# Kernel tuning notes

Measured on AMD Instinct MI355X. Metric: run time of the kernel, lower is better.

The kernel has to match this reference:

```python
import jax, jax.numpy as jnp
import numpy as np

N_HEAD = 16

def setup_inputs() -> dict:
    key = jax.random.key(0)
    k1, k2, k3 = jax.random.split(key, 3)
    B, T, C = 2, 2048, 2048
    x = jax.random.normal(k1, (B, T, C), dtype=jnp.float32)
    # torch Linear weights are [out, in]; init with small scale for stability
    w_attn = jax.random.normal(k2, (3 * C, C), dtype=jnp.float32) * 0.02
    b_attn = jnp.zeros((3 * C,), dtype=jnp.float32)
    w_proj = jax.random.normal(k3, (C, C), dtype=jnp.float32) * 0.02
    b_proj = jnp.zeros((C,), dtype=jnp.float32)
    return {"x": x, "w_attn": w_attn, "b_attn": b_attn, "w_proj": w_proj, "b_proj": b_proj}

def reference(x, w_attn, b_attn, w_proj, b_proj):
    B, T, C = x.shape
    nh = N_HEAD
    hs = C // nh
    # fused QKV projection (torch Linear: x @ W^T + b)
    qkv = x @ w_attn.T + b_attn                      # [B, T, 3C]
    q, k, v = jnp.split(qkv, 3, axis=2)
    # [B, nh, T, hs]
    q = q.reshape(B, T, nh, hs).transpose(0, 2, 1, 3)
    k = k.reshape(B, T, nh, hs).transpose(0, 2, 1, 3)
    v = v.reshape(B, T, nh, hs).transpose(0, 2, 1, 3)
    # causal scaled dot-product attention
    scale = 1.0 / jnp.sqrt(jnp.asarray(hs, dtype=x.dtype))
    logits = jnp.einsum("bhqd,bhkd->bhqk", q, k) * scale  # [B, nh, T, T]
    causal = jnp.tril(jnp.ones((T, T), dtype=bool))
    logits = jnp.where(causal, logits, jnp.finfo(logits.dtype).min)
    attn = jax.nn.softmax(logits, axis=-1)
    y = jnp.einsum("bhqk,bhkd->bhqd", attn, v)       # [B, nh, T, hs]
    y = y.transpose(0, 2, 1, 3).reshape(B, T, C)
    # output projection (resid_dropout is identity in eval / p=0)
    y = y @ w_proj.T + b_proj
    return y
```

## Files before the change

### kernel.cpp

```cpp
#include <hip/hip_runtime.h>
#include <stdint.h>

typedef __bf16 bf16_t;
typedef __bf16 bf16x8 __attribute__((ext_vector_type(8)));
typedef float f32x4 __attribute__((ext_vector_type(4)));
typedef unsigned short us16x8 __attribute__((ext_vector_type(8)));

#define MFMA16(a, b, c) __builtin_amdgcn_mfma_f32_16x16x32_bf16(a, b, c, 0, 0, 0)
#define BAR() __builtin_amdgcn_s_barrier()
#define PRIO1() __builtin_amdgcn_s_setprio(1)
#define PRIO0() __builtin_amdgcn_s_setprio(0)
#define LGKM0()                                        \
  do {                                                 \
    asm volatile("s_waitcnt lgkmcnt(0)" ::: "memory"); \
    __builtin_amdgcn_sched_barrier(0);                 \
  } while (0)
#define VMCNT(n)                                          \
  do {                                                    \
    asm volatile("s_waitcnt vmcnt(" #n ")" ::: "memory"); \
    __builtin_amdgcn_sched_barrier(0);                    \
  } while (0)

__device__ __forceinline__ void stage16(const bf16_t* g, bf16_t* l) {
  __builtin_amdgcn_global_load_lds((__attribute__((address_space(1))) void*)g,
                                   (__attribute__((address_space(3))) void*)l, 16, 0, 0);
}

__global__ __launch_bounds__(256) void cvt_f32_to_bf16(const float* __restrict__ in,
                                                       bf16_t* __restrict__ out, int n8) {
  int i = blockIdx.x * 256 + threadIdx.x;
  if (i >= n8) return;
  const f32x4* p = (const f32x4*)(in + (size_t)i * 8);
  f32x4 a = p[0], b = p[1];
  bf16x8 o;
  o[0] = (bf16_t)a[0]; o[1] = (bf16_t)a[1]; o[2] = (bf16_t)a[2]; o[3] = (bf16_t)a[3];
  o[4] = (bf16_t)b[0]; o[5] = (bf16_t)b[1]; o[6] = (bf16_t)b[2]; o[7] = (bf16_t)b[3];
  *(bf16x8*)(out + (size_t)i * 8) = o;
}

template <int OUT_BF16>
__global__ __launch_bounds__(256, 2) void gemm_w128p(const bf16_t* __restrict__ A,
                                                     const bf16_t* __restrict__ B,
                                                     const float* __restrict__ bias,
                                                     void* __restrict__ Cout,
                                                     int M, int N, int K) {
  __shared__ bf16_t SA[3 * 256 * 32];
  __shared__ bf16_t SB[3 * 128 * 32];
  const int tid = threadIdx.x;
  const int l = tid & 63, w = tid >> 6;
  const int l15 = l & 15, l4 = l >> 4;
  const int wm = w >> 1, wn = w & 1;
  const int nbn = N >> 7;
  const int nbm = M >> 8;
  const int total = nbm * nbn;
  const int bnpc = nbn >> 3;

  const int r0 = tid >> 2;
  const int scol = (((tid & 3) ^ ((r0 >> 1) & 3)) << 3);
  const size_t K64 = (size_t)64 * K;

  const int swz = (l4 ^ ((l15 >> 1) & 3)) << 3;
  int aoff[8], boff[4];
#pragma unroll
  for (int i = 0; i < 8; ++i) aoff[i] = (wm * 128 + i * 16 + l15) * 32 + swz;
#pragma unroll
  for (int i = 0; i < 4; ++i) boff[i] = (wn * 64 + i * 16 + l15) * 32 + swz;

  const int nk = K >> 5;

  for (int wk = blockIdx.x; wk < total; wk += gridDim.x) {
    const int c = wk & 7, rr0 = wk >> 3;
    const int bm = rr0 / bnpc;
    const int bn = c * bnpc + rr0 % bnpc;

    const bf16_t* gA = A + (size_t)(bm * 256 + r0) * K + scol;
    const bf16_t* gB = B + (size_t)(bn * 128 + r0) * K + scol;

    f32x4 acc[8][4] = {};

    auto STAGE = [&](int t2, int buf) {
      const size_t ko = (size_t)t2 * 32;
      stage16(gA + ko, SA + buf * 8192 + tid * 8);
      stage16(gA + K64 + ko, SA + buf * 8192 + 2048 + tid * 8);
      stage16(gA + 2 * K64 + ko, SA + buf * 8192 + 4096 + tid * 8);
      stage16(gA + 3 * K64 + ko, SA + buf * 8192 + 6144 + tid * 8);
      stage16(gB + ko, SB + buf * 4096 + tid * 8);
      stage16(gB + K64 + ko, SB + buf * 4096 + 2048 + tid * 8);
    };

    auto TILE = [&](int t, int bufR, int bufS) {
      const int t2 = (t + 2 < nk) ? t + 2 : nk - 1;
      STAGE(t2, bufS);
      bf16x8 aR[8], bR[4];
#pragma unroll
      for (int i = 0; i < 8; ++i) aR[i] = *(const bf16x8*)(SA + bufR * 8192 + aoff[i]);
#pragma unroll
      for (int i = 0; i < 4; ++i) bR[i] = *(const bf16x8*)(SB + bufR * 4096 + boff[i]);
      VMCNT(6);
      BAR();
      LGKM0();
      PRIO1();
#pragma unroll
      for (int mi = 0; mi < 8; ++mi)
#pragma unroll
        for (int ni = 0; ni < 4; ++ni)
          acc[mi][ni] = MFMA16(aR[mi], bR[ni], acc[mi][ni]);
      PRIO0();
      BAR();
    };

    STAGE(0, 0);
    STAGE(1, 1);
    VMCNT(6);
    BAR();

    for (int t = 0; t < nk - 1; t += 3) {
      TILE(t, 0, 2);
      TILE(t + 1, 1, 0);
      TILE(t + 2, 2, 1);
    }
    TILE(nk - 1, 0, 2);
    VMCNT(0);

    const int rbase = bm * 256 + wm * 128 + (l4 << 2);
    const int cbase = bn * 128 + wn * 64 + l15;
#pragma unroll
    for (int ni = 0; ni < 4; ++ni) {
      float bv = bias[cbase + ni * 16];
#pragma unroll
      for (int mi = 0; mi < 8; ++mi)
#pragma unroll
        for (int rr = 0; rr < 4; ++rr) {
          float v = acc[mi][ni][rr] + bv;
          size_t off = (size_t)(rbase + mi * 16 + rr) * N + (cbase + ni * 16);
          if (OUT_BF16) ((bf16_t*)Cout)[off] = (bf16_t)v;
          else ((float*)Cout)[off] = v;
        }
    }
  }
}

template <int OUT_BF16>
__global__ __launch_bounds__(256, 3) void gemm_tb3(const bf16_t* __restrict__ A,
                                                   const bf16_t* __restrict__ B,
                                                   const float* __restrict__ bias,
                                                   void* __restrict__ Cout,
                                                   int M, int N, int K) {
  __shared__ bf16_t SA[3 * 128 * 32];
  __shared__ bf16_t SB[3 * 128 * 32];
  const int tid = threadIdx.x;
  const int l = tid & 63, w = tid >> 6;
  const int l15 = l & 15, l4 = l >> 4;
  const int wm = w >> 1, wn = w & 1;
  const int nbm = M >> 7;
  const int nwg = gridDim.x;
  const int bid = blockIdx.x;
  const int wg = (bid & 7) * (nwg >> 3) + (bid >> 3);
  const int bn = wg / nbm, bm = wg % nbm;

  const int r0 = tid >> 2;
  const int sc = (((tid & 3) ^ ((r0 >> 1) & 3)) << 3);
  const bf16_t* gA = A + (size_t)(bm * 128 + r0) * K + sc;
  const bf16_t* gB = B + (size_t)(bn * 128 + r0) * K + sc;
  const size_t rowK64 = (size_t)64 * K;

  const int swz = (l4 ^ ((l15 >> 1) & 3)) << 3;
  int aoff[4], boff[4];
#pragma unroll
  for (int i = 0; i < 4; ++i) {
    aoff[i] = (wm * 64 + i * 16 + l15) * 32 + swz;
    boff[i] = (wn * 64 + i * 16 + l15) * 32 + swz;
  }

  f32x4 acc[4][4] = {};
  const int nk = K >> 5;

  auto STAGE = [&](int t2, int buf) {
    const size_t ko = (size_t)t2 * 32;
    stage16(gA + ko, SA + buf * 4096 + tid * 8);
    stage16(gA + rowK64 + ko, SA + buf * 4096 + 2048 + tid * 8);
    stage16(gB + ko, SB + buf * 4096 + tid * 8);
    stage16(gB + rowK64 + ko, SB + buf * 4096 + 2048 + tid * 8);
  };

  auto TILE = [&](int t, int bufR, int bufS) {
    const int t2 = (t + 2 < nk) ? t + 2 : nk - 1;
    STAGE(t2, bufS);
    bf16x8 aR[4], bR[4];
#pragma unroll
    for (int i = 0; i < 4; ++i) {
      aR[i] = *(const bf16x8*)(SA + bufR * 4096 + aoff[i]);
      bR[i] = *(const bf16x8*)(SB + bufR * 4096 + boff[i]);
    }
    VMCNT(4);
    BAR();
    LGKM0();
    PRIO1();
#pragma unroll
    for (int mi = 0; mi < 4; ++mi)
#pragma unroll
      for (int ni = 0; ni < 4; ++ni)
        acc[mi][ni] = MFMA16(aR[mi], bR[ni], acc[mi][ni]);
    PRIO0();
    BAR();
  };

  STAGE(0, 0);
  STAGE(1, 1);
  VMCNT(4);
  BAR();

  for (int t = 0; t < nk - 1; t += 3) {
    TILE(t, 0, 2);
    TILE(t + 1, 1, 0);
    TILE(t + 2, 2, 1);
  }
  TILE(nk - 1, 0, 2);
  VMCNT(0);

  const int rbase = bm * 128 + wm * 64 + (l4 << 2);
  const int cbase = bn * 128 + wn * 64 + l15;
#pragma unroll
  for (int ni = 0; ni < 4; ++ni) {
    float bv = bias[cbase + ni * 16];
#pragma unroll
    for (int mi = 0; mi < 4; ++mi)
#pragma unroll
      for (int r = 0; r < 4; ++r) {
        float v = acc[mi][ni][r] + bv;
        size_t off = (size_t)(rbase + mi * 16 + r) * N + (cbase + ni * 16);
        if (OUT_BF16) ((bf16_t*)Cout)[off] = (bf16_t)v;
        else ((float*)Cout)[off] = v;
      }
  }
}

__global__ __launch_bounds__(256, 2) void attn_fwd(const bf16_t* __restrict__ qkv,
                                                   bf16_t* __restrict__ att) {
  __shared__ bf16_t Kt[64 * 128];
  __shared__ bf16_t Vt[128 * 64];
  __shared__ bf16_t Pw[4][16 * 64];

  int bid = blockIdx.x;
  int pair = bid >> 5, bh = bid & 31;
  int h = bh & 15, b = bh >> 4;
  int tid = threadIdx.x;
  int l = tid & 63, w = tid >> 6;
  int l15 = l & 15, l4 = l >> 4, l7 = l & 7;
  const size_t LD = 6144;
  const bf16_t* base = qkv + (size_t)b * 2048 * LD;

#pragma unroll 1
  for (int phase = 0; phase < 2; ++phase) {
    int qt = phase ? 31 - pair : pair;
    int q0 = qt << 6;
    int wq0 = q0 + w * 16;

    bf16x8 qf[4];
#pragma unroll
    for (int kk = 0; kk < 4; ++kk)
      qf[kk] = *(const bf16x8*)(base + (size_t)(wq0 + l15) * LD + h * 128 + kk * 32 + l4 * 8);

    f32x4 acc[8] = {};
    float mrow[4], lrow[4];
#pragma unroll
    for (int r = 0; r < 4; ++r) { mrow[r] = -1e30f; lrow[r] = 0.f; }

    int nkt = qt + 1;
    for (int kt = 0; kt < nkt; ++kt) {
      int kb = kt << 6;
      const bf16_t* vg = base + (size_t)kb * LD + 4096 + h * 128;
      us16x8 va[2], vb[2];
#pragma unroll
      for (int p = 0; p < 2; ++p) {
        int g = p * 256 + tid;
        int kv = (g >> 4) << 1;
        int d0 = (g & 15) << 3;
        va[p] = *(const us16x8*)(vg + (size_t)kv * LD + d0);
        vb[p] = *(const us16x8*)(vg + (size_t)(kv + 1) * LD + d0);
      }
      const bf16_t* kg = base + (size_t)kb * LD + 2048 + h * 128;
#pragma unroll
      for (int i = 0; i < 4; ++i) {
        int e = i * 256 + tid;
        int row = e >> 4, blk = e & 15;
        int src = (blk ^ (row & 7)) << 3;
        stage16(kg + (size_t)row * LD + src, Kt + e * 8);
      }
#pragma unroll
      for (int p = 0; p < 2; ++p) {
        int g = p * 256 + tid;
        int kv = (g >> 4) << 1;
        int d0 = (g & 15) << 3;
        int k8 = kv >> 3, kr = kv & 7;
#pragma unroll
        for (int j = 0; j < 8; ++j) {
          int d = d0 + j;
          int swz = k8 ^ ((d ^ (d >> 3)) & 7);
          unsigned pack = (unsigned)va[p][j] | ((unsigned)vb[p][j] << 16);
          *(unsigned*)(&Vt[d * 64 + swz * 8 + kr]) = pack;
        }
      }
      __syncthreads();

      {
        f32x4 s[4] = {};
        __builtin_amdgcn_s_setprio(1);
#pragma unroll
        for (int kk = 0; kk < 4; ++kk) {
          int blk = (kk * 4 + l4) ^ l7;
#pragma unroll
          for (int n = 0; n < 4; ++n) {
            bf16x8 kf = *(const bf16x8*)(Kt + (n * 16 + l15) * 128 + blk * 8);
            s[n] = MFMA16(qf[kk], kf, s[n]);
          }
        }
        __builtin_amdgcn_s_setprio(0);

        const float sc = 0.08838834764831845f;
        bool needMask = (kb + 63) > wq0;
        float scf[4];
#pragma unroll
        for (int r = 0; r < 4; ++r) {
          int q = wq0 + (l4 << 2) + r;
#pragma unroll
          for (int n = 0; n < 4; ++n) {
            float v = s[n][r] * sc;
            if (needMask && (kb + n * 16 + l15) > q) v = -1e30f;
            s[n][r] = v;
          }
          float mx = fmaxf(fmaxf(s[0][r], s[1][r]), fmaxf(s[2][r], s[3][r]));
          mx = fmaxf(mx, __shfl_xor(mx, 1));
          mx = fmaxf(mx, __shfl_xor(mx, 2));
          mx = fmaxf(mx, __shfl_xor(mx, 4));
          mx = fmaxf(mx, __shfl_xor(mx, 8));
          float mn = fmaxf(mrow[r], mx);
          float sf = __expf(mrow[r] - mn);
          mrow[r] = mn;
          scf[r] = sf;
          float rs = 0.f;
#pragma unroll
          for (int n = 0; n < 4; ++n) {
            float pv = __expf(s[n][r] - mn);
            s[n][r] = pv;
            rs += pv;
          }
          rs += __shfl_xor(rs, 1);
          rs += __shfl_xor(rs, 2);
          rs += __shfl_xor(rs, 4);
          rs += __shfl_xor(rs, 8);
          lrow[r] = lrow[r] * sf + rs;
        }
#pragma unroll
        for (int nd = 0; nd < 8; ++nd)
#pragma unroll
          for (int r = 0; r < 4; ++r)
            acc[nd][r] *= scf[r];
#pragma unroll
        for (int n = 0; n < 4; ++n) {
          int cb8 = n * 2 + (l15 >> 3);
#pragma unroll
          for (int r = 0; r < 4; ++r) {
            int row = (l4 << 2) + r;
            Pw[w][row * 64 + ((cb8 ^ (row & 7)) << 3) + l7] = (bf16_t)s[n][r];
          }
        }
        __builtin_amdgcn_s_setprio(1);
#pragma unroll
        for (int kk2 = 0; kk2 < 2; ++kk2) {
          bf16x8 pa = *(const bf16x8*)(&Pw[w][l15 * 64 + (((kk2 * 4 + l4) ^ l7) << 3)]);
#pragma unroll
          for (int nd = 0; nd < 8; ++nd) {
            int d = nd * 16 + l15;
            int swz = (kk2 * 4 + l4) ^ ((d ^ (d >> 3)) & 7);
            bf16x8 bv = *(const bf16x8*)(&Vt[d * 64 + swz * 8]);
            acc[nd] = MFMA16(pa, bv, acc[nd]);
          }
        }
        __builtin_amdgcn_s_setprio(0);
      }
      __syncthreads();
    }

#pragma unroll
    for (int r = 0; r < 4; ++r) {
      float inv = 1.0f / lrow[r];
      size_t ro = (size_t)(b * 2048 + wq0 + (l4 << 2) + r) * 2048 + h * 128;
#pragma unroll
      for (int nd = 0; nd < 8; ++nd)
        att[ro + nd * 16 + l15] = (bf16_t)(acc[nd][r] * inv);
    }
  }
}

extern "C" void kernel_launch(void* const* d_in, const int* in_sizes, int n_in,
                              void* d_out, int out_size, void* d_ws, size_t ws_size,
                              hipStream_t stream) {
  (void)in_sizes; (void)n_in; (void)out_size; (void)ws_size;
  const float* x = (const float*)d_in[0];
  const float* w_attn = (const float*)d_in[1];
  const float* b_attn = (const float*)d_in[2];
  const float* w_proj = (const float*)d_in[3];
  const float* b_proj = (const float*)d_in[4];
  float* out = (float*)d_out;

  char* ws = (char*)d_ws;
  bf16_t* xb  = (bf16_t*)(ws);
  bf16_t* wab = (bf16_t*)(ws + 16777216);
  bf16_t* wpb = (bf16_t*)(ws + 41943040);
  bf16_t* qkv = (bf16_t*)(ws + 50331648);
  bf16_t* att = xb;

  cvt_f32_to_bf16<<<4096, 256, 0, stream>>>(x, xb, 1048576);
  cvt_f32_to_bf16<<<6144, 256, 0, stream>>>(w_attn, wab, 1572864);
  cvt_f32_to_bf16<<<2048, 256, 0, stream>>>(w_proj, wpb, 524288);

  gemm_w128p<1><<<512, 256, 0, stream>>>(xb, wab, b_attn, qkv, 4096, 6144, 2048);

  attn_fwd<<<512, 256, 0, stream>>>(qkv, att);

  gemm_tb3<0><<<512, 256, 0, stream>>>(att, wpb, b_proj, out, 4096, 2048, 2048);
}
```

Before: 286.7 us.

## Use 512-thread 256x192 tile GEMM for QKV and wide-tile GEMM for projection

Adds a new QKV GEMM kernel with 512 threads (8 waves) computing 256x192 output tiles. It runs 256 blocks that each make two passes over a block-swizzled tile order, with conditional staging of the B tile and per-wave vmcnt waits. The output projection now uses the existing 256x128 gemm_w128p kernel instead of the 128x128 gemm_tb3 kernel. The larger tiles should raise arithmetic intensity and cut LDS and global traffic per FLOP. The cost is more register pressure and fewer blocks in flight, so occupancy and tail effects may suffer.

```diff
diff --git a/kernel.cpp b/kernel.cpp
--- a/kernel.cpp
+++ b/kernel.cpp
@@ -36,6 +36,103 @@
   o[0] = (bf16_t)a[0]; o[1] = (bf16_t)a[1]; o[2] = (bf16_t)a[2]; o[3] = (bf16_t)a[3];
   o[4] = (bf16_t)b[0]; o[5] = (bf16_t)b[1]; o[6] = (bf16_t)b[2]; o[7] = (bf16_t)b[3];
   *(bf16x8*)(out + (size_t)i * 8) = o;
+}
+
+template <int OUT_BF16>
+__global__ __launch_bounds__(512, 2) void gemm_wide(const bf16_t* __restrict__ A,
+                                                    const bf16_t* __restrict__ B,
+                                                    const float* __restrict__ bias,
+                                                    void* __restrict__ Cout,
+                                                    int M, int N, int K) {
+  __shared__ bf16_t SA[3 * 256 * 32];
+  __shared__ bf16_t SB[3 * 192 * 32];
+  const int tid = threadIdx.x;
+  const int l = tid & 63, w = tid >> 6;
+  const int l15 = l & 15, l4 = l >> 4;
+  const int wm = w >> 2, wn = w & 3;
+  const bool w4 = (tid < 256);
+  const int nk = K >> 5;
+
+  const int r0 = tid >> 2;
+  const int sc = (((tid & 3) ^ ((r0 >> 1) & 3)) << 3);
+  const size_t K128 = (size_t)128 * K;
+
+  const int swz = (l4 ^ ((l15 >> 1) & 3)) << 3;
+  int aoff[8], boff[3];
+#pragma unroll
+  for (int i = 0; i < 8; ++i) aoff[i] = (wm * 128 + i * 16 + l15) * 32 + swz;
+#pragma unroll
+  for (int i = 0; i < 3; ++i) boff[i] = (wn * 48 + i * 16 + l15) * 32 + swz;
+
+#pragma unroll 1
+  for (int pass = 0; pass < 2; ++pass) {
+    const int T = 64 * (blockIdx.x & 7) + (blockIdx.x >> 3) + 32 * pass;
+    const int c = T >> 6, loc = T & 63;
+    const int bn = 4 * c + (loc >> 4), bm = loc & 15;
+
+    const bf16_t* gA = A + (size_t)(bm * 256 + r0) * K + sc;
+    const bf16_t* gB = B + (size_t)(bn * 192 + r0) * K + sc;
+
+    f32x4 acc[8][3] = {};
+
+    auto STAGE = [&](int t2, int buf) {
+      const size_t ko = (size_t)t2 * 32;
+      stage16(gA + ko, SA + buf * 8192 + tid * 8);
+      stage16(gA + K128 + ko, SA + buf * 8192 + 4096 + tid * 8);
+      stage16(gB + ko, SB + buf * 6144 + tid * 8);
+      if (w4) stage16(gB + K128 + ko, SB + buf * 6144 + 4096 + tid * 8);
+    };
+
+    auto TILE = [&](int t, int bufR, int bufS) {
+      const int t2 = (t + 2 < nk) ? t + 2 : nk - 1;
+      STAGE(t2, bufS);
+      bf16x8 aR[8], bR[3];
+#pragma unroll
+      for (int i = 0; i < 8; ++i) aR[i] = *(const bf16x8*)(SA + bufR * 8192 + aoff[i]);
+#pragma unroll
+      for (int i = 0; i < 3; ++i) bR[i] = *(const bf16x8*)(SB + bufR * 6144 + boff[i]);
+      if (w4) { VMCNT(4); } else { VMCNT(3); }
+      BAR();
+      LGKM0();
+      PRIO1();
+#pragma unroll
+      for (int mi = 0; mi < 8; ++mi)
+#pragma unroll
+        for (int ni = 0; ni < 3; ++ni)
+          acc[mi][ni] = MFMA16(aR[mi], bR[ni], acc[mi][ni]);
+      PRIO0();
+      BAR();
+    };
+
+    STAGE(0, 0);
+    STAGE(1, 1);
+    if (w4) { VMCNT(4); } else { VMCNT(3); }
+    BAR();
+
+    for (int t = 0; t < nk - 1; t += 3) {
+      TILE(t, 0, 2);
+      TILE(t + 1, 1, 0);
+      TILE(t + 2, 2, 1);
+    }
+    TILE(nk - 1, 0, 2);
+    VMCNT(0);
+
+    const int rbase = bm * 256 + wm * 128 + (l4 << 2);
+    const int cbase = bn * 192 + wn * 48 + l15;
+#pragma unroll
+    for (int ni = 0; ni < 3; ++ni) {
+      float bv = bias[cbase + ni * 16];
+#pragma unroll
+      for (int mi = 0; mi < 8; ++mi)
+#pragma unroll
+        for (int rr = 0; rr < 4; ++rr) {
+          float v = acc[mi][ni][rr] + bv;
+          size_t off = (size_t)(rbase + mi * 16 + rr) * N + (cbase + ni * 16);
+          if (OUT_BF16) ((bf16_t*)Cout)[off] = (bf16_t)v;
+          else ((float*)Cout)[off] = v;
+        }
+    }
+  }
 }
 
 template <int OUT_BF16>
@@ -140,101 +237,6 @@
   }
 }
 
-template <int OUT_BF16>
-__global__ __launch_bounds__(256, 3) void gemm_tb3(const bf16_t* __restrict__ A,
-                                                   const bf16_t* __restrict__ B,
-                                                   const float* __restrict__ bias,
-                                                   void* __restrict__ Cout,
-                                                   int M, int N, int K) {
-  __shared__ bf16_t SA[3 * 128 * 32];
-  __shared__ bf16_t SB[3 * 128 * 32];
-  const int tid = threadIdx.x;
-  const int l = tid & 63, w = tid >> 6;
-  const int l15 = l & 15, l4 = l >> 4;
-  const int wm = w >> 1, wn = w & 1;
-  const int nbm = M >> 7;
-  const int nwg = gridDim.x;
-  const int bid = blockIdx.x;
-  const int wg = (bid & 7) * (nwg >> 3) + (bid >> 3);
-  const int bn = wg / nbm, bm = wg % nbm;
-
-  const int r0 = tid >> 2;
-  const int sc = (((tid & 3) ^ ((r0 >> 1) & 3)) << 3);
-  const bf16_t* gA = A + (size_t)(bm * 128 + r0) * K + sc;
-  const bf16_t* gB = B + (size_t)(bn * 128 + r0) * K + sc;
-  const size_t rowK64 = (size_t)64 * K;
-
-  const int swz = (l4 ^ ((l15 >> 1) & 3)) << 3;
-  int aoff[4], boff[4];
-#pragma unroll
-  for (int i = 0; i < 4; ++i) {
-    aoff[i] = (wm * 64 + i * 16 + l15) * 32 + swz;
-    boff[i] = (wn * 64 + i * 16 + l15) * 32 + swz;
-  }
-
-  f32x4 acc[4][4] = {};
-  const int nk = K >> 5;
-
-  auto STAGE = [&](int t2, int buf) {
-    const size_t ko = (size_t)t2 * 32;
-    stage16(gA + ko, SA + buf * 4096 + tid * 8);
-    stage16(gA + rowK64 + ko, SA + buf * 4096 + 2048 + tid * 8);
-    stage16(gB + ko, SB + buf * 4096 + tid * 8);
-    stage16(gB + rowK64 + ko, SB + buf * 4096 + 2048 + tid * 8);
-  };
-
-  auto TILE = [&](int t, int bufR, int bufS) {
-    const int t2 = (t + 2 < nk) ? t + 2 : nk - 1;
-    STAGE(t2, bufS);
-    bf16x8 aR[4], bR[4];
-#pragma unroll
-    for (int i = 0; i < 4; ++i) {
-      aR[i] = *(const bf16x8*)(SA + bufR * 4096 + aoff[i]);
-      bR[i] = *(const bf16x8*)(SB + bufR * 4096 + boff[i]);
-    }
-    VMCNT(4);
-    BAR();
-    LGKM0();
-    PRIO1();
-#pragma unroll
-    for (int mi = 0; mi < 4; ++mi)
-#pragma unroll
-      for (int ni = 0; ni < 4; ++ni)
-        acc[mi][ni] = MFMA16(aR[mi], bR[ni], acc[mi][ni]);
-    PRIO0();
-    BAR();
-  };
-
-  STAGE(0, 0);
-  STAGE(1, 1);
-  VMCNT(4);
-  BAR();
-
-  for (int t = 0; t < nk - 1; t += 3) {
-    TILE(t, 0, 2);
-    TILE(t + 1, 1, 0);
-    TILE(t + 2, 2, 1);
-  }
-  TILE(nk - 1, 0, 2);
-  VMCNT(0);
-
-  const int rbase = bm * 128 + wm * 64 + (l4 << 2);
-  const int cbase = bn * 128 + wn * 64 + l15;
-#pragma unroll
-  for (int ni = 0; ni < 4; ++ni) {
-    float bv = bias[cbase + ni * 16];
-#pragma unroll
-    for (int mi = 0; mi < 4; ++mi)
-#pragma unroll
-      for (int r = 0; r < 4; ++r) {
-        float v = acc[mi][ni][r] + bv;
-        size_t off = (size_t)(rbase + mi * 16 + r) * N + (cbase + ni * 16);
-        if (OUT_BF16) ((bf16_t*)Cout)[off] = (bf16_t)v;
-        else ((float*)Cout)[off] = v;
-      }
-  }
-}
-
 __global__ __launch_bounds__(256, 2) void attn_fwd(const bf16_t* __restrict__ qkv,
                                                    bf16_t* __restrict__ att) {
   __shared__ bf16_t Kt[64 * 128];
@@ -415,9 +417,9 @@
   cvt_f32_to_bf16<<<6144, 256, 0, stream>>>(w_attn, wab, 1572864);
   cvt_f32_to_bf16<<<2048, 256, 0, stream>>>(w_proj, wpb, 524288);
 
-  gemm_w128p<1><<<512, 256, 0, stream>>>(xb, wab, b_attn, qkv, 4096, 6144, 2048);
+  gemm_wide<1><<<256, 512, 0, stream>>>(xb, wab, b_attn, qkv, 4096, 6144, 2048);
 
   attn_fwd<<<512, 256, 0, stream>>>(qkv, att);
 
-  gemm_tb3<0><<<512, 256, 0, stream>>>(att, wpb, b_proj, out, 4096, 2048, 2048);
-}
+  gemm_w128p<0><<<512, 256, 0, stream>>>(att, wpb, b_proj, out, 4096, 2048, 2048);
+}
```

New measurement: 320.8 us. 11.9% more time.
